# Optimization experiments

Hardware: AMD Instinct MI355X
Metric: run time of the kernel (lower is better)

The kernel has to match this reference:

```python
import jax, jax.numpy as jnp
import numpy as np

B, IN_C, IN_L, T = 8, 64, 64, 256
OUT_C, OUT_L = 64, 64
KH, KW = 3, 3
K = IN_C * KH * KW  # 576
EPS = 1e-5


def setup_inputs() -> dict:
    key = jax.random.key(0)
    k1, k2 = jax.random.split(key, 2)
    x = jax.random.normal(k1, (B, IN_C, IN_L, T), dtype=jnp.float32)
    # xavier-normal-ish scale for fan_in = K
    weight = jax.random.normal(k2, (K, OUT_C, OUT_L), dtype=jnp.float32) * (1.0 / np.sqrt(K))
    bias = jnp.zeros((OUT_C, OUT_L), dtype=jnp.float32)
    gamma = jnp.ones((OUT_C,), dtype=jnp.float32)
    beta = jnp.zeros((OUT_C,), dtype=jnp.float32)
    alpha = jnp.full((1,), 0.25, dtype=jnp.float32)  # PReLU single-parameter init
    return {"x": x, "weight": weight, "bias": bias, "gamma": gamma, "beta": beta, "alpha": alpha}


def _unfold3x3(x):
    # torch nn.Unfold(kernel=(3,3), stride=1, padding=1): output channel index = c*9 + i*3 + j
    xp = jnp.pad(x, ((0, 0), (0, 0), (1, 1), (1, 1)))
    pats = jnp.stack([xp[:, :, i:i + IN_L, j:j + T] for i in range(KH) for j in range(KW)], axis=2)  # (B, C, 9, L, T)
    return pats.reshape(x.shape[0], K, IN_L, T)


def reference(x, weight, bias, gamma, beta, alpha):
    patches = _unfold3x3(x)  # (B, K, L, T); out_l_unfold == in_l, out_t == t, so slicing is a no-op
    # locally-connected conv: per out_l position weight, shared over time
    out = jnp.einsum('bklt,kcl->bclt', patches, weight)  # (B, out_c, out_l, T)
    out = out + bias[None, :, :, None]
    # BatchNorm2d (training mode: batch statistics, biased variance)
    mean = out.mean(axis=(0, 2, 3), keepdims=True)
    var = out.var(axis=(0, 2, 3), keepdims=True)
    out = (out - mean) * jax.lax.rsqrt(var + EPS) * gamma[None, :, None, None] + beta[None, :, None, None]
    # PReLU with single shared parameter
    return jnp.where(out >= 0, out, alpha[0] * out)
```

## Files before the change

kernel.cpp:

```cpp
#include <hip/hip_runtime.h>

typedef __attribute__((ext_vector_type(8))) short short8;
typedef __attribute__((ext_vector_type(8))) unsigned short ushort8;
typedef __attribute__((ext_vector_type(4))) float f32x4;

constexpr int B_ = 8, IN_C_ = 64, IN_L_ = 64, T_ = 256, OUT_C_ = 64, OUT_L_ = 64;
constexpr float EPS_ = 1e-5f;

constexpr int XT_LP = 66, XT_TP = 258, XT_IC = 64;
constexpr int XT_LSTRIDE = XT_TP * XT_IC;
constexpr int XT_BSTRIDE = XT_LP * XT_LSTRIDE;
constexpr size_t XT_ELEMS = (size_t)B_ * XT_BSTRIDE;
constexpr size_t XT_BYTES = XT_ELEMS * 2;
constexpr size_t WT2_ELEMS = 64ull * 9 * 64 * 64;
constexpr size_t WT2_OFF_B = XT_BYTES;
constexpr size_t PART_OFF_B = WT2_OFF_B + WT2_ELEMS * 2;
constexpr size_t PART_BYTES = 512ull * 128 * 4;
constexpr size_t TMP_OFF_B = PART_OFF_B + PART_BYTES;
constexpr size_t TMP_BYTES = (size_t)B_ * OUT_C_ * OUT_L_ * T_ * 2;
constexpr size_t WS_NEED = TMP_OFF_B;
constexpr size_t WS_NEED2 = TMP_OFF_B + TMP_BYTES;

__device__ __forceinline__ unsigned short f2bf(float f) {
  unsigned u = __float_as_uint(f);
  return (unsigned short)((u + 0x7fffu + ((u >> 16) & 1u)) >> 16);
}

__device__ __forceinline__ void gload_lds16(const void* g, void* l) {
  __builtin_amdgcn_global_load_lds(
      (const __attribute__((address_space(1))) unsigned int*)g,
      (__attribute__((address_space(3))) unsigned int*)l, 16, 0, 0);
}

__global__ __launch_bounds__(256) void prep_kernel(const float* __restrict__ x,
                                                   const float* __restrict__ w,
                                                   unsigned short* __restrict__ xT,
                                                   unsigned short* __restrict__ wT2) {
  const int bid = blockIdx.x;
  const int tid = threadIdx.x;
  __shared__ unsigned char shmem[34816];
  if (bid < 144) {
    const int tap = bid >> 4;
    const int c0 = (bid & 15) * 4;
    auto wls = (unsigned short(*)[4][68])shmem;
    {
      const int ic = tid >> 2, cl = tid & 3;
      const float* src = w + (((size_t)(ic * 9 + tap) * 64) + (c0 + cl)) * 64;
#pragma unroll
      for (int e = 0; e < 16; ++e) {
        float4 v = ((const float4*)src)[e];
        const int l = e * 4;
        wls[l + 0][cl][ic] = f2bf(v.x);
        wls[l + 1][cl][ic] = f2bf(v.y);
        wls[l + 2][cl][ic] = f2bf(v.z);
        wls[l + 3][cl][ic] = f2bf(v.w);
      }
    }
    __syncthreads();
    {
      const int l = tid >> 2, cl = tid & 3;
      const unsigned short* row = &wls[l][cl][0];
      uint4* dst = (uint4*)(wT2 + ((size_t)(l * 9 + tap)) * 4096 + (c0 + cl) * 64);
#pragma unroll
      for (int q = 0; q < 8; ++q) dst[q] = ((const uint4*)row)[q];
    }
  } else if (bid < 1168) {
    const int u = bid - 144;
    const int th = u & 1, l = (u >> 1) & 63, b = u >> 7;
    const int t0 = th * 128;
    auto ls = (unsigned short(*)[132])shmem;
    {
      const int ic = tid >> 2, q = tid & 3;
      const float4* src = (const float4*)(x + (((size_t)(b * 64 + ic) * 64 + l) * 256 + t0));
#pragma unroll
      for (int e = 0; e < 8; ++e) {
        float4 v = src[q * 8 + e];
        const int toff = (q * 8 + e) * 4;
        unsigned d0 = f2bf(v.x) | ((unsigned)f2bf(v.y) << 16);
        unsigned d1 = f2bf(v.z) | ((unsigned)f2bf(v.w) << 16);
        *(uint2*)&ls[ic][toff] = make_uint2(d0, d1);
      }
    }
    __syncthreads();
    {
      const int tl = tid >> 1, h = tid & 1;
      unsigned d[16];
#pragma unroll
      for (int k = 0; k < 16; ++k) {
        unsigned short a = ls[h * 32 + 2 * k][tl];
        unsigned short c = ls[h * 32 + 2 * k + 1][tl];
        d[k] = a | ((unsigned)c << 16);
      }
      unsigned short* dst =
          xT + ((size_t)(b * XT_LP + l + 1) * XT_TP + (t0 + tl + 1)) * XT_IC + h * 32;
      uint4* dv = (uint4*)dst;
      dv[0] = make_uint4(d[0], d[1], d[2], d[3]);
      dv[1] = make_uint4(d[4], d[5], d[6], d[7]);
      dv[2] = make_uint4(d[8], d[9], d[10], d[11]);
      dv[3] = make_uint4(d[12], d[13], d[14], d[15]);
    }
  } else {
    const int b = bid - 1168;
    unsigned short* base = xT + (size_t)b * XT_BSTRIDE;
    const short8 z = {};
    for (int ci = tid; ci < 5184; ci += 256) {
      size_t off;
      if (ci < 4128) {
        const int plane = ci / 2064, k = ci % 2064;
        off = (size_t)(plane ? 65 : 0) * XT_LSTRIDE + (size_t)k * 8;
      } else {
        const int k = ci - 4128;
        const int lp = k >> 4, rem = k & 15;
        const int tp = (rem < 8) ? 0 : 257;
        off = ((size_t)lp * XT_TP + tp) * 64 + (size_t)(rem & 7) * 8;
      }
      *(short8*)(base + off) = z;
    }
  }
}

__global__ __launch_bounds__(256, 2) void conv_mfma(
    const unsigned short* __restrict__ xT, const unsigned short* __restrict__ wT2,
    const float* __restrict__ bias, float* __restrict__ outf,
    unsigned short* __restrict__ tmpb, float* __restrict__ part) {
  const int orig = blockIdx.x;
  const int wg = (orig >> 6) * 64 + (orig & 7) * 8 + ((orig >> 3) & 7);
  const int b = wg >> 6, l = wg & 63;
  const int tid = threadIdx.x;
  const int wid = tid >> 6, ln = tid & 63;
  const int lc = ln & 15, lg = ln >> 4;
  const int m0 = wid * 64;

  __shared__ unsigned short lds[2][20480];

  const int src_lane_off = ((ln >> 3) << 6) + ((((ln & 7) ^ (ln >> 3))) << 3);
  const unsigned short* xBase = xT + (size_t)(b * XT_LP + l) * XT_LSTRIDE + src_lane_off;
  const unsigned short* wBase = wT2 + (size_t)l * 9 * 4096 + src_lane_off;

  auto STAGE = [&](int buf, int tap) {
    const int i = tap / 3, j = tap - i * 3;
    const unsigned short* Ab = xBase + (size_t)i * XT_LSTRIDE + j * 64;
    unsigned short* La = &lds[buf][0];
#pragma unroll
    for (int q = 0; q < 8; ++q) {
      const int ch = wid * 8 + q;
      gload_lds16(Ab + ch * 512, La + ch * 512);
    }
    const unsigned short* Bb = wBase + (size_t)tap * 4096;
    unsigned short* Lb = &lds[buf][16384];
#pragma unroll
    for (int q = 0; q < 2; ++q) {
      const int ch = wid * 2 + q;
      gload_lds16(Bb + ch * 512, Lb + ch * 512);
    }
  };

  f32x4 acc[4][4] = {};

  STAGE(0, 0);
#pragma unroll
  for (int tap = 0; tap < 9; ++tap) {
    __builtin_amdgcn_s_barrier();
    if (tap + 1 < 9) {
      STAGE((tap + 1) & 1, tap + 1);
      asm volatile("s_waitcnt vmcnt(10)" ::: "memory");
    } else {
      asm volatile("s_waitcnt vmcnt(0)" ::: "memory");
    }
    __builtin_amdgcn_sched_barrier(0);
    __builtin_amdgcn_s_barrier();
    __builtin_amdgcn_sched_barrier(0);

    const unsigned short* La = &lds[tap & 1][0];
    const unsigned short* Lb = &lds[tap & 1][16384];
#pragma unroll
    for (int kb = 0; kb < 2; ++kb) {
      const int slot = (((kb * 4 + lg) ^ (lc & 7)) << 3);
      short8 af[4], bf[4];
#pragma unroll
      for (int mi = 0; mi < 4; ++mi)
        af[mi] = *(const short8*)(La + (m0 + mi * 16 + lc) * 64 + slot);
#pragma unroll
      for (int ni = 0; ni < 4; ++ni)
        bf[ni] = *(const short8*)(Lb + (ni * 16 + lc) * 64 + slot);
#pragma unroll
      for (int mi = 0; mi < 4; ++mi)
#pragma unroll
        for (int ni = 0; ni < 4; ++ni)
          acc[mi][ni] =
              __builtin_amdgcn_mfma_f32_16x16x32_bf16(af[mi], bf[ni], acc[mi][ni], 0, 0, 0);
    }
  }

  __syncthreads();
  float* sm = (float*)&lds[0][0];
#pragma unroll
  for (int ni = 0; ni < 4; ++ni) {
    const int c = ni * 16 + lc;
    const float bv = bias[c * 64 + l];
    float s = 0.f, s2 = 0.f;
    const size_t obase = ((size_t)(b * 64 + c) * 64 + l) * 256 + m0;
#pragma unroll
    for (int mi = 0; mi < 4; ++mi) {
      float vv[4];
#pragma unroll
      for (int r = 0; r < 4; ++r) {
        float v = acc[mi][ni][r] + bv;
        vv[r] = v;
        s += v;
        s2 += v * v;
      }
      if (tmpb) {
        unsigned d0 = f2bf(vv[0]) | ((unsigned)f2bf(vv[1]) << 16);
        unsigned d1 = f2bf(vv[2]) | ((unsigned)f2bf(vv[3]) << 16);
        *(uint2*)(tmpb + obase + mi * 16 + lg * 4) = make_uint2(d0, d1);
      } else {
        *(float4*)(outf + obase + mi * 16 + lg * 4) =
            make_float4(vv[0], vv[1], vv[2], vv[3]);
      }
    }
    s += __shfl_xor(s, 16);  s += __shfl_xor(s, 32);
    s2 += __shfl_xor(s2, 16); s2 += __shfl_xor(s2, 32);
    if (lg == 0) {
      sm[(wid * 4 + ni) * 32 + lc * 2] = s;
      sm[(wid * 4 + ni) * 32 + lc * 2 + 1] = s2;
    }
  }
  __syncthreads();
  if (tid < 128) {
    const int sel = tid >> 6, cc = tid & 63;
    const int ni = cc >> 4, lc2 = cc & 15;
    float r = 0.f;
#pragma unroll
    for (int w2 = 0; w2 < 4; ++w2) r += sm[(w2 * 4 + ni) * 32 + lc2 * 2 + sel];
    part[(size_t)wg * 128 + sel * 64 + cc] = r;
  }
}

__global__ __launch_bounds__(256) void bn_stats_prelu_b(
    const float* __restrict__ part, const float* __restrict__ gamma,
    const float* __restrict__ beta, const float* __restrict__ alpha,
    const unsigned short* __restrict__ tmp, float* __restrict__ out) {
  const int c = blockIdx.x >> 5;
  const int seg = blockIdx.x & 31;
  const int tid = threadIdx.x;
  float s = 0.f, s2 = 0.f;
  for (int i = tid; i < 512; i += 256) {
    s += part[(size_t)i * 128 + c];
    s2 += part[(size_t)i * 128 + 64 + c];
  }
#pragma unroll
  for (int off = 32; off; off >>= 1) {
    s += __shfl_down(s, off);
    s2 += __shfl_down(s2, off);
  }
  __shared__ float r0[4], r1[4];
  const int wid = tid >> 6, lane = tid & 63;
  if (lane == 0) { r0[wid] = s; r1[wid] = s2; }
  __syncthreads();
  const float S = r0[0] + r0[1] + r0[2] + r0[3];
  const float S2 = r1[0] + r1[1] + r1[2] + r1[3];
  const float inv_n = 1.0f / 131072.f;
  const float mean = S * inv_n;
  const float var = S2 * inv_n - mean * mean;
  const float sc = gamma[c] * rsqrtf(var + EPS_);
  const float sh = beta[c] - mean * sc;
  const float a = alpha[0];
  const size_t base8 = ((size_t)((seg >> 2) * 64 + c)) * 2048 + (size_t)(seg & 3) * 512;
#pragma unroll 2
  for (int k = tid; k < 512; k += 256) {
    const size_t i = base8 + k;
    ushort8 v = *(const ushort8*)(tmp + i * 8);
    float o[8];
#pragma unroll
    for (int r = 0; r < 8; ++r) {
      float f = __uint_as_float(((unsigned)v[r]) << 16) * sc + sh;
      o[r] = (f >= 0.f) ? f : a * f;
    }
    float4* op = (float4*)(out + i * 8);
    op[0] = make_float4(o[0], o[1], o[2], o[3]);
    op[1] = make_float4(o[4], o[5], o[6], o[7]);
  }
}

__global__ __launch_bounds__(256) void bn_stats_prelu_f(
    const float* __restrict__ part, const float* __restrict__ gamma,
    const float* __restrict__ beta, const float* __restrict__ alpha,
    float* __restrict__ out) {
  const int c = blockIdx.x >> 5;
  const int seg = blockIdx.x & 31;
  const int tid = threadIdx.x;
  float s = 0.f, s2 = 0.f;
  for (int i = tid; i < 512; i += 256) {
    s += part[(size_t)i * 128 + c];
    s2 += part[(size_t)i * 128 + 64 + c];
  }
#pragma unroll
  for (int off = 32; off; off >>= 1) {
    s += __shfl_down(s, off);
    s2 += __shfl_down(s2, off);
  }
  __shared__ float r0[4], r1[4];
  const int wid = tid >> 6, lane = tid & 63;
  if (lane == 0) { r0[wid] = s; r1[wid] = s2; }
  __syncthreads();
  const float S = r0[0] + r0[1] + r0[2] + r0[3];
  const float S2 = r1[0] + r1[1] + r1[2] + r1[3];
  const float inv_n = 1.0f / 131072.f;
  const float mean = S * inv_n;
  const float var = S2 * inv_n - mean * mean;
  const float sc = gamma[c] * rsqrtf(var + EPS_);
  const float sh = beta[c] - mean * sc;
  const float a = alpha[0];
  const size_t base4 = ((size_t)((seg >> 2) * 64 + c)) * 4096 + (size_t)(seg & 3) * 1024;
  for (int k = tid; k < 1024; k += 256) {
    float4 v = ((float4*)out)[base4 + k];
    v.x = v.x * sc + sh; v.x = (v.x >= 0.f) ? v.x : a * v.x;
    v.y = v.y * sc + sh; v.y = (v.y >= 0.f) ? v.y : a * v.y;
    v.z = v.z * sc + sh; v.z = (v.z >= 0.f) ? v.z : a * v.z;
    v.w = v.w * sc + sh; v.w = (v.w >= 0.f) ? v.w : a * v.w;
    ((float4*)out)[base4 + k] = v;
  }
}

extern "C" void kernel_launch(void* const* d_in, const int* in_sizes, int n_in,
                              void* d_out, int out_size, void* d_ws, size_t ws_size,
                              hipStream_t stream) {
  const float* x = (const float*)d_in[0];
  const float* w = (const float*)d_in[1];
  const float* bias = (const float*)d_in[2];
  const float* gamma = (const float*)d_in[3];
  const float* beta = (const float*)d_in[4];
  const float* alpha = (const float*)d_in[5];
  float* out = (float*)d_out;

  unsigned short* xT = (unsigned short*)d_ws;
  unsigned short* wT2 = (unsigned short*)((char*)d_ws + WT2_OFF_B);
  float* part = (float*)((char*)d_ws + PART_OFF_B);

  if (ws_size >= WS_NEED2) {
    unsigned short* tmpb = (unsigned short*)((char*)d_ws + TMP_OFF_B);
    prep_kernel<<<dim3(1176), dim3(256), 0, stream>>>(x, w, xT, wT2);
    conv_mfma<<<dim3(512), dim3(256), 0, stream>>>(xT, wT2, bias, out, tmpb, part);
    bn_stats_prelu_b<<<dim3(2048), dim3(256), 0, stream>>>(part, gamma, beta, alpha, tmpb, out);
  } else if (ws_size >= WS_NEED) {
    prep_kernel<<<dim3(1176), dim3(256), 0, stream>>>(x, w, xT, wT2);
    conv_mfma<<<dim3(512), dim3(256), 0, stream>>>(xT, wT2, bias, out, nullptr, part);
    bn_stats_prelu_f<<<dim3(2048), dim3(256), 0, stream>>>(part, gamma, beta, alpha, out);
  }
}
```

Before: 53.42 us.

## Stage each padded input row once and reuse it across the three horizontal taps

The conv kernel no longer copies a fresh 256x64 A tile into LDS for each of the nine taps. It now loads one whole padded time row (258 positions) per vertical tap `i`. The three horizontal taps `j` read that row at shifted offsets with a matching XOR swizzle, so global-to-LDS traffic for the input drops threefold and LDS use shrinks. Only the weight tile stays double-buffered. The cost is that each next-row load happens after a barrier at the end of `j==2` and is not prefetched, so its latency is exposed twice per block.

```diff
diff --git a/kernel.cpp b/kernel.cpp
--- a/kernel.cpp
+++ b/kernel.cpp
@@ -131,39 +131,45 @@
   const int lc = ln & 15, lg = ln >> 4;
   const int m0 = wid * 64;
 
-  __shared__ unsigned short lds[2][20480];
+  __shared__ unsigned short Arow[18432];
+  __shared__ unsigned short Bl[2][4096];
 
   const int src_lane_off = ((ln >> 3) << 6) + ((((ln & 7) ^ (ln >> 3))) << 3);
-  const unsigned short* xBase = xT + (size_t)(b * XT_LP + l) * XT_LSTRIDE + src_lane_off;
   const unsigned short* wBase = wT2 + (size_t)l * 9 * 4096 + src_lane_off;
-
-  auto STAGE = [&](int buf, int tap) {
-    const int i = tap / 3, j = tap - i * 3;
-    const unsigned short* Ab = xBase + (size_t)i * XT_LSTRIDE + j * 64;
-    unsigned short* La = &lds[buf][0];
-#pragma unroll
-    for (int q = 0; q < 8; ++q) {
-      const int ch = wid * 8 + q;
-      gload_lds16(Ab + ch * 512, La + ch * 512);
-    }
+  const unsigned short* xRow0 = xT + (size_t)(b * XT_LP + l) * XT_LSTRIDE;
+
+  auto ASTAGE = [&](int i) {
+    const unsigned short* rb = xRow0 + (size_t)i * XT_LSTRIDE;
+#pragma unroll
+    for (int k = 0; k < 9; ++k) {
+      const int cbase = k * 256 + wid * 64;
+      const int ci = cbase + ln;
+      const int tp = ci >> 3, s = ci & 7;
+      gload_lds16(rb + tp * 64 + ((s ^ (tp & 7)) << 3), Arow + (size_t)cbase * 8);
+    }
+  };
+  auto BSTAGE = [&](int buf, int tap) {
     const unsigned short* Bb = wBase + (size_t)tap * 4096;
-    unsigned short* Lb = &lds[buf][16384];
 #pragma unroll
     for (int q = 0; q < 2; ++q) {
       const int ch = wid * 2 + q;
-      gload_lds16(Bb + ch * 512, Lb + ch * 512);
+      gload_lds16(Bb + ch * 512, &Bl[buf][0] + ch * 512);
     }
   };
 
   f32x4 acc[4][4] = {};
 
-  STAGE(0, 0);
+  ASTAGE(0);
+  BSTAGE(0, 0);
+  __syncthreads();
+
 #pragma unroll
   for (int tap = 0; tap < 9; ++tap) {
+    const int i = tap / 3, j = tap - i * 3;
     __builtin_amdgcn_s_barrier();
     if (tap + 1 < 9) {
-      STAGE((tap + 1) & 1, tap + 1);
-      asm volatile("s_waitcnt vmcnt(10)" ::: "memory");
+      BSTAGE((tap + 1) & 1, tap + 1);
+      asm volatile("s_waitcnt vmcnt(2)" ::: "memory");
     } else {
       asm volatile("s_waitcnt vmcnt(0)" ::: "memory");
     }
@@ -171,18 +177,19 @@
     __builtin_amdgcn_s_barrier();
     __builtin_amdgcn_sched_barrier(0);
 
-    const unsigned short* La = &lds[tap & 1][0];
-    const unsigned short* Lb = &lds[tap & 1][16384];
+    const unsigned short* Lb = &Bl[tap & 1][0];
 #pragma unroll
     for (int kb = 0; kb < 2; ++kb) {
-      const int slot = (((kb * 4 + lg) ^ (lc & 7)) << 3);
+      const int q = kb * 4 + lg;
       short8 af[4], bf[4];
 #pragma unroll
-      for (int mi = 0; mi < 4; ++mi)
-        af[mi] = *(const short8*)(La + (m0 + mi * 16 + lc) * 64 + slot);
+      for (int mi = 0; mi < 4; ++mi) {
+        const int tp = m0 + mi * 16 + lc + j;
+        af[mi] = *(const short8*)(Arow + tp * 64 + ((q ^ (tp & 7)) << 3));
+      }
 #pragma unroll
       for (int ni = 0; ni < 4; ++ni)
-        bf[ni] = *(const short8*)(Lb + (ni * 16 + lc) * 64 + slot);
+        bf[ni] = *(const short8*)(Lb + (ni * 16 + lc) * 64 + ((q ^ (lc & 7)) << 3));
 #pragma unroll
       for (int mi = 0; mi < 4; ++mi)
 #pragma unroll
@@ -190,10 +197,15 @@
           acc[mi][ni] =
               __builtin_amdgcn_mfma_f32_16x16x32_bf16(af[mi], bf[ni], acc[mi][ni], 0, 0, 0);
     }
-  }
-
-  __syncthreads();
-  float* sm = (float*)&lds[0][0];
+
+    if (j == 2 && i < 2) {
+      __builtin_amdgcn_s_barrier();
+      ASTAGE(i + 1);
+    }
+  }
+
+  __syncthreads();
+  float* sm = (float*)&Arow[0];
 #pragma unroll
   for (int ni = 0; ni < 4; ++ni) {
     const int c = ni * 16 + lc;
```

Result: faster. 51.68 us, median of 2 (-3.3%).
